# Kernel tuning notes

Measured on AMD Instinct MI355X. Metric: run time of the kernel, lower is better.

## Reference

```python
import jax, jax.numpy as jnp
import numpy as np

DEPTH = 256
SEQ = 394
EMB = 300


def _branch(x_nch, W, b, n):
    # W: [depth, n*EMB], flatten order of paragraph[i:i+n,:].flatten() is (time, emb)
    k = W.reshape(DEPTH, n, EMB).transpose(0, 2, 1)  # OIH: [depth, EMB, n]
    y = jax.lax.conv_general_dilated(
        x_nch, k, window_strides=(1,), padding='VALID',
        dimension_numbers=('NCH', 'OIH', 'NCH'))  # [B, depth, SEQ-n+1]
    # original loop only covers windows i = 0 .. SEQ-n-1 (SEQ-n windows)
    y = y[:, :, :SEQ - n] + b  # b: [depth, 1] broadcasts over time
    # running max starts at 0 and relu clamps >= 0; outer relu is a no-op
    return jnp.max(jax.nn.relu(y), axis=-1)  # [B, depth]


def setup_inputs() -> dict:
    key = jax.random.key(0)
    ks = jax.random.split(key, 7)
    inp = {
        'input': jax.random.normal(ks[0], (64, SEQ, EMB), dtype=jnp.float32),
        'W1': jax.random.normal(ks[1], (DEPTH, 3 * EMB), dtype=jnp.float32),
        'W2': jax.random.normal(ks[2], (DEPTH, 4 * EMB), dtype=jnp.float32),
        'W3': jax.random.normal(ks[3], (DEPTH, 5 * EMB), dtype=jnp.float32),
        'b1': jax.random.normal(ks[4], (DEPTH, 1), dtype=jnp.float32),
        'b2': jax.random.normal(ks[5], (DEPTH, 1), dtype=jnp.float32),
        'b3': jax.random.normal(ks[6], (DEPTH, 1), dtype=jnp.float32),
    }
    return inp


def reference(input, W1, W2, W3, b1, b2, b3):
    x = input.transpose(0, 2, 1)  # [B, EMB, SEQ] (NCH)
    o1 = _branch(x, W1, b1, 3)
    o2 = _branch(x, W2, b2, 4)
    o3 = _branch(x, W3, b3, 5)
    return jnp.concatenate([o1, o2, o3], axis=1)  # [B, 3*depth]
```

## Files before the change

kernel.cpp:

```cpp
#include <hip/hip_runtime.h>
#include <hip/hip_bf16.h>

#define SEQ 394
#define EMB 300
#define EMBP 312
#define NROWS (64 * SEQ)
#define XPTOT ((long)NROWS * EMBP)
#define NCHT 118
#define CBE0 29
#define CBE1 68
#define XELEM 41472

typedef __attribute__((ext_vector_type(8))) short short8;
typedef __attribute__((ext_vector_type(4))) float f32x4;

__device__ __forceinline__ unsigned short f2b(float f) {
    unsigned u = __float_as_uint(f);
    u += 0x7FFFu + ((u >> 16) & 1u);
    return (unsigned short)(u >> 16);
}

__device__ __forceinline__ void gload_lds16(const void* g, void* l) {
    __builtin_amdgcn_global_load_lds(
        (const __attribute__((address_space(1))) void*)g,
        (__attribute__((address_space(3))) void*)l, 16, 0, 0);
}


__global__ __launch_bounds__(256)
void pack_x_kernel(const float* __restrict__ x, unsigned short* __restrict__ xp)
{
    long q = (long)blockIdx.x * 256 + threadIdx.x;
    int row = (int)(q / 78);
    int c4  = ((int)(q - (long)row * 78)) * 4;
    ushort4 u;
    if (c4 < 300) {
        float4 v = *(const float4*)(x + (long)row * 300 + c4);
        u = make_ushort4(f2b(v.x), f2b(v.y), f2b(v.z), f2b(v.w));
    } else {
        u = make_ushort4(0, 0, 0, 0);
    }
    *(ushort4*)(xp + q * 4) = u;
}

__global__ __launch_bounds__(256)
void pack_w_kernel(const float* __restrict__ W1, const float* __restrict__ W2,
                   const float* __restrict__ W3, unsigned short* __restrict__ wb)
{
    int G = blockIdx.x * 256 + threadIdx.x;
    int l  = G & 63;
    int g  = (G >> 6) & 15;
    int c  = G >> 10;
    const float* Wg; int n, cb;
    if (c <= CBE0)      { Wg = W1; n = 3; cb = 0;        }
    else if (c <= CBE1) { Wg = W2; n = 4; cb = CBE0 + 1; }
    else                { Wg = W3; n = 5; cb = CBE1 + 1; }
    const int K = n * 300;
    const int f = g * 16 + (l & 15);
    const int kl = (c - cb) * 32 + (l >> 4) * 8;
    unsigned short v[8];
#pragma unroll
    for (int j = 0; j < 8; ++j) {
        int kk = kl + j;
        int r  = kk / EMBP;
        int e  = kk - r * EMBP;
        v[j] = (r < n && e < 300) ? f2b(Wg[(long)f * K + r * 300 + e]) : (unsigned short)0;
    }
    unsigned short* dst = wb + (long)G * 8;
    *(ushort4*)dst       = make_ushort4(v[0], v[1], v[2], v[3]);
    *(ushort4*)(dst + 4) = make_ushort4(v[4], v[5], v[6], v[7]);
}


__global__ __launch_bounds__(1024, 1)
void convgemm_kernel(const unsigned short* __restrict__ xp,
                     const unsigned short* __restrict__ wb,
                     const float* __restrict__ b1, const float* __restrict__ b2,
                     const float* __restrict__ b3,
                     float* __restrict__ out)
{
    __shared__ unsigned short X[XELEM];

    const int tid  = threadIdx.x;
    const int lane = tid & 63;
    const int wid  = tid >> 6;
    const int wfs  = wid >> 1;
    const int ws   = wid & 1;
    const int lr   = lane & 15, lg = lane >> 4;
    const int b    = blockIdx.x >> 2;
    const int ti   = blockIdx.x & 3;
    const int woff = (ti == 0) ? 0 : (ti == 1) ? 88 : (ti == 2) ? 176 : 263;

    {
        const long xbase = ((long)b * SEQ + woff) * EMBP;
        const long slim  = XPTOT - 8;
#pragma unroll
        for (int rd = 0; rd < 6; ++rd) {
            int gbase = rd * 1024 + wid * 64;
            if (gbase < 5184) {
                long se = xbase + (long)(gbase + lane) * 8;
                if (se > slim) se = slim;
                gload_lds16(xp + se, &X[gbase * 8]);
            }
        }
    }
    __syncthreads();

    const unsigned short* wp0 = wb + ((long)(wfs * 2) * 64 + lane) * 8;
    auto LDW = [&](int c, short8 (&w)[2]) {
        const short8* p = (const short8*)(wp0 + (long)c * 8192);
        w[0] = p[0];
        w[1] = p[64];
    };

    const unsigned short* xr = &X[(ws * 64 + lr) * EMBP + lg * 8];
    auto RDBX = [&](int ko, short8 (&bx)[4]) {
        bx[0] = *(const short8*)(xr + ko);
        bx[1] = *(const short8*)(xr + ko + 16 * EMBP);
        bx[2] = *(const short8*)(xr + ko + 32 * EMBP);
        bx[3] = *(const short8*)(xr + ko + 48 * EMBP);
    };

    auto MFMA8 = [&](const short8 (&w)[2], const short8 (&bx)[4], f32x4 (&acc)[2][4]) {
#pragma unroll
        for (int mi = 0; mi < 2; ++mi)
#pragma unroll
            for (int ni = 0; ni < 4; ++ni)
                acc[mi][ni] = __builtin_amdgcn_mfma_f32_16x16x32_bf16(w[mi], bx[ni], acc[mi][ni], 0, 0, 0);
    };

    auto EPI = [&](int br, f32x4 (&acc)[2][4]) {
        const float* bg = (br == 0) ? b1 : (br == 1) ? b2 : b3;
        const int Nw = 391 - br;
        const int ob = b * 768 + br * 256;
#pragma unroll
        for (int mi = 0; mi < 2; ++mi) {
#pragma unroll
            for (int r = 0; r < 4; ++r) {
                const int d = wfs * 32 + mi * 16 + lg * 4 + r;
                const float bv = bg[d];
                float m = 0.f;
#pragma unroll
                for (int ni = 0; ni < 4; ++ni) {
                    int w = woff + ws * 64 + ni * 16 + lr;
                    float v = fmaxf(acc[mi][ni][r] + bv, 0.f);
                    if (w >= Nw) v = 0.f;
                    m = fmaxf(m, v);
                }
#pragma unroll
                for (int off = 1; off < 16; off <<= 1)
                    m = fmaxf(m, __shfl_xor(m, off));
                if (lr == 0)
                    atomicMax((int*)(out + ob + d), __float_as_int(m));
            }
        }
#pragma unroll
        for (int i = 0; i < 2; ++i)
#pragma unroll
            for (int j = 0; j < 4; ++j)
                acc[i][j] = (f32x4)0.0f;
    };

    f32x4 accA[2][4], accB[2][4];
#pragma unroll
    for (int i = 0; i < 2; ++i)
#pragma unroll
        for (int j = 0; j < 4; ++j) {
            accA[i][j] = (f32x4)0.0f;
            accB[i][j] = (f32x4)0.0f;
        }

    short8 w1A[2], w1B[2], w2A[2], w2B[2], bx[4];

    LDW(30, w1A); LDW(69, w2A);
    LDW(31, w1B); LDW(70, w2B);
    for (int j = 0; j < 38; j += 2) {
        RDBX(j * 32, bx);
        MFMA8(w1A, bx, accA);
        MFMA8(w2A, bx, accB);
        { int t = (j + 2 < 39) ? j + 2 : 38; LDW(30 + t, w1A); LDW(69 + t, w2A); }

        RDBX((j + 1) * 32, bx);
        MFMA8(w1B, bx, accA);
        MFMA8(w2B, bx, accB);
        { int t = (j + 3 < 39) ? j + 3 : 38; LDW(30 + t, w1B); LDW(69 + t, w2B); }
    }
    RDBX(38 * 32, bx);
    MFMA8(w1A, bx, accA);
    MFMA8(w2A, bx, accB);

    LDW(69 + 39, w2A); LDW(69 + 40, w2B);
    EPI(1, accA);

    for (int t = 0; t < 10; t += 2) {
        RDBX((39 + t) * 32, bx);
        MFMA8(w2A, bx, accB);
        { int u = (41 + t < 49) ? 41 + t : 48; LDW(69 + u, w2A); }

        RDBX((40 + t) * 32, bx);
        MFMA8(w2B, bx, accB);
        { int u = (42 + t < 49) ? 42 + t : 48; LDW(69 + u, w2B); }
    }

    LDW(0, w1A); LDW(1, w1B);
    EPI(2, accB);

    for (int j = 0; j < 30; j += 2) {
        RDBX(j * 32, bx);
        MFMA8(w1A, bx, accA);
        { int t = (j + 2 < 30) ? j + 2 : 29; LDW(t, w1A); }

        RDBX((j + 1) * 32, bx);
        MFMA8(w1B, bx, accA);
        { int t = (j + 3 < 30) ? j + 3 : 29; LDW(t, w1B); }
    }
    EPI(0, accA);
}


__device__ __forceinline__ void load_chunk(const float* __restrict__ Wg,
                                           const float* __restrict__ xb,
                                           int K, int dbase, int i0, int k0, int tid,
                                           float4 wv[4], float4 xv[4])
{
#pragma unroll
    for (int i = 0; i < 4; ++i) {
        int fi  = tid + (i << 8);
        int row = fi >> 3;
        int c4  = (fi & 7) << 2;
        int col = k0 + c4;
        if (col < K)
            wv[i] = *(const float4*)(Wg + (long)(dbase + row) * K + col);
        else
            wv[i] = make_float4(0.f, 0.f, 0.f, 0.f);
        int off = (i0 + row) * EMB + col;
        int lim = SEQ * EMB - 4;
        if (off > lim) off = lim;
        xv[i] = *(const float4*)(xb + off);
    }
}

__device__ __forceinline__ void write_chunk(unsigned short (*Wb)[40],
                                            unsigned short (*Xb)[40],
                                            int tid, const float4 wv[4], const float4 xv[4])
{
#pragma unroll
    for (int i = 0; i < 4; ++i) {
        int fi  = tid + (i << 8);
        int row = fi >> 3;
        int c4  = (fi & 7) << 2;
        *(ushort4*)&Wb[row][c4] = make_ushort4(f2b(wv[i].x), f2b(wv[i].y), f2b(wv[i].z), f2b(wv[i].w));
        *(ushort4*)&Xb[row][c4] = make_ushort4(f2b(xv[i].x), f2b(xv[i].y), f2b(xv[i].z), f2b(xv[i].w));
    }
}

__global__ __launch_bounds__(256, 2)
void convmax_fallback(const float* __restrict__ x,
                      const float* __restrict__ W1, const float* __restrict__ W2,
                      const float* __restrict__ W3,
                      const float* __restrict__ b1, const float* __restrict__ b2,
                      const float* __restrict__ b3,
                      float* __restrict__ out)
{
    const int br = blockIdx.z;
    const int K  = (br == 0) ? 900 : (br == 1) ? 1200 : 1500;
    const int Nw = SEQ - 3 - br;
    const float* Wg = (br == 0) ? W1 : (br == 1) ? W2 : W3;
    const float* bg = (br == 0) ? b1 : (br == 1) ? b2 : b3;
    const int b  = blockIdx.x;
    const int mt = blockIdx.y >> 2;
    const int nt = blockIdx.y & 3;
    const int dbase = mt * 128;
    const int i0    = nt * 128;
    const float* xb = x + b * (SEQ * EMB);
    const int nch = (K + 31) >> 5;

    __shared__ unsigned short Wl[2][128][40];
    __shared__ unsigned short Xl[2][128][40];

    const int tid  = threadIdx.x;
    const int lane = tid & 63;
    const int wid  = tid >> 6;
    const int wr = wid >> 1, wc = wid & 1;
    const int lr = lane & 15, lg = lane >> 4;

    f32x4 acc[4][4];
#pragma unroll
    for (int i = 0; i < 4; ++i)
#pragma unroll
        for (int j = 0; j < 4; ++j)
            acc[i][j] = (f32x4)0.0f;

    {
        float4 wv[4], xv[4];
        load_chunk(Wg, xb, K, dbase, i0, 0, tid, wv, xv);
        write_chunk(Wl[0], Xl[0], tid, wv, xv);
    }
    __syncthreads();

    for (int c = 0; c < nch; ++c) {
        const int cur = c & 1;
        float4 wv[4], xv[4];
        const bool pf = (c + 1 < nch);
        if (pf) load_chunk(Wg, xb, K, dbase, i0, (c + 1) << 5, tid, wv, xv);

        short8 af[4], bfr[4];
#pragma unroll
        for (int mi = 0; mi < 4; ++mi)
            af[mi] = *(const short8*)&Wl[cur][wr * 64 + mi * 16 + lr][lg * 8];
#pragma unroll
        for (int ni = 0; ni < 4; ++ni)
            bfr[ni] = *(const short8*)&Xl[cur][wc * 64 + ni * 16 + lr][lg * 8];
#pragma unroll
        for (int mi = 0; mi < 4; ++mi)
#pragma unroll
            for (int ni = 0; ni < 4; ++ni)
                acc[mi][ni] = __builtin_amdgcn_mfma_f32_16x16x32_bf16(af[mi], bfr[ni], acc[mi][ni], 0, 0, 0);

        if (pf) write_chunk(Wl[cur ^ 1], Xl[cur ^ 1], tid, wv, xv);
        __syncthreads();
    }

    const int ob = b * 768 + br * 256;
#pragma unroll
    for (int mi = 0; mi < 4; ++mi) {
#pragma unroll
        for (int rI = 0; rI < 4; ++rI) {
            const int d = dbase + wr * 64 + mi * 16 + lg * 4 + rI;
            const float bv = bg[d];
            float m = 0.f;
#pragma unroll
            for (int ni = 0; ni < 4; ++ni) {
                int win = i0 + wc * 64 + ni * 16 + lr;
                float v = acc[mi][ni][rI] + bv;
                v = fmaxf(v, 0.f);
                if (win >= Nw) v = 0.f;
                m = fmaxf(m, v);
            }
#pragma unroll
            for (int off = 1; off < 16; off <<= 1)
                m = fmaxf(m, __shfl_xor(m, off));
            if (lr == 0)
                atomicMax((int*)(out + ob + d), __float_as_int(m));
        }
    }
}


extern "C" void kernel_launch(void* const* d_in, const int* in_sizes, int n_in,
                              void* d_out, int out_size, void* d_ws, size_t ws_size,
                              hipStream_t stream) {
    const float* x  = (const float*)d_in[0];
    const float* W1 = (const float*)d_in[1];
    const float* W2 = (const float*)d_in[2];
    const float* W3 = (const float*)d_in[3];
    const float* b1 = (const float*)d_in[4];
    const float* b2 = (const float*)d_in[5];
    const float* b3 = (const float*)d_in[6];
    float* out = (float*)d_out;

    hipMemsetAsync(d_out, 0, (size_t)out_size * sizeof(float), stream);

    const long WBTOT = (long)NCHT * 8192;
    const size_t need = (size_t)(XPTOT + WBTOT) * 2;

    if (ws_size >= need) {
        unsigned short* xp = (unsigned short*)d_ws;
        unsigned short* wbb = xp + XPTOT;

        pack_x_kernel<<<7683, 256, 0, stream>>>(x, xp);
        pack_w_kernel<<<472, 256, 0, stream>>>(W1, W2, W3, wbb);
        convgemm_kernel<<<256, 1024, 0, stream>>>(xp, wbb, b1, b2, b3, out);
    } else {
        dim3 grid(64, 8, 3);
        convmax_fallback<<<grid, 256, 0, stream>>>(x, W1, W2, W3, b1, b2, b3, out);
    }
}
```

Before: 85.00 us.

## Fuse input bf16 packing into conv GEMM and restructure MFMA software pipeline

```diff
diff --git a/kernel.cpp b/kernel.cpp
--- a/kernel.cpp
+++ b/kernel.cpp
@@ -5,11 +5,11 @@
 #define EMB 300
 #define EMBP 312
 #define NROWS (64 * SEQ)
-#define XPTOT ((long)NROWS * EMBP)
 #define NCHT 118
 #define CBE0 29
 #define CBE1 68
 #define XELEM 41472
+#define XGR 5148
 
 typedef __attribute__((ext_vector_type(8))) short short8;
 typedef __attribute__((ext_vector_type(4))) float f32x4;
@@ -20,28 +20,6 @@
     return (unsigned short)(u >> 16);
 }
 
-__device__ __forceinline__ void gload_lds16(const void* g, void* l) {
-    __builtin_amdgcn_global_load_lds(
-        (const __attribute__((address_space(1))) void*)g,
-        (__attribute__((address_space(3))) void*)l, 16, 0, 0);
-}
-
-
-__global__ __launch_bounds__(256)
-void pack_x_kernel(const float* __restrict__ x, unsigned short* __restrict__ xp)
-{
-    long q = (long)blockIdx.x * 256 + threadIdx.x;
-    int row = (int)(q / 78);
-    int c4  = ((int)(q - (long)row * 78)) * 4;
-    ushort4 u;
-    if (c4 < 300) {
-        float4 v = *(const float4*)(x + (long)row * 300 + c4);
-        u = make_ushort4(f2b(v.x), f2b(v.y), f2b(v.z), f2b(v.w));
-    } else {
-        u = make_ushort4(0, 0, 0, 0);
-    }
-    *(ushort4*)(xp + q * 4) = u;
-}
 
 __global__ __launch_bounds__(256)
 void pack_w_kernel(const float* __restrict__ W1, const float* __restrict__ W2,
@@ -73,7 +51,7 @@
 
 
 __global__ __launch_bounds__(1024, 1)
-void convgemm_kernel(const unsigned short* __restrict__ xp,
+void convgemm_kernel(const float* __restrict__ x,
                      const unsigned short* __restrict__ wb,
                      const float* __restrict__ b1, const float* __restrict__ b2,
                      const float* __restrict__ b3,
@@ -91,27 +69,42 @@
     const int ti   = blockIdx.x & 3;
     const int woff = (ti == 0) ? 0 : (ti == 1) ? 88 : (ti == 2) ? 176 : 263;
 
-    {
-        const long xbase = ((long)b * SEQ + woff) * EMBP;
-        const long slim  = XPTOT - 8;
-#pragma unroll
-        for (int rd = 0; rd < 6; ++rd) {
-            int gbase = rd * 1024 + wid * 64;
-            if (gbase < 5184) {
-                long se = xbase + (long)(gbase + lane) * 8;
-                if (se > slim) se = slim;
-                gload_lds16(xp + se, &X[gbase * 8]);
-            }
-        }
-    }
-    __syncthreads();
-
     const unsigned short* wp0 = wb + ((long)(wfs * 2) * 64 + lane) * 8;
     auto LDW = [&](int c, short8 (&w)[2]) {
         const short8* p = (const short8*)(wp0 + (long)c * 8192);
         w[0] = p[0];
         w[1] = p[64];
     };
+
+    short8 w1[2], w2[2];
+    LDW(30, w1); LDW(69, w2);
+
+    {
+        const float* xs = x + ((long)b * SEQ + woff) * 300;
+        const long growbase = (long)b * SEQ + woff;
+#pragma unroll
+        for (int rd = 0; rd < 6; ++rd) {
+            int gi = rd * 1024 + tid;
+            if (gi < XGR) {
+                int row = gi / 39;
+                int g   = gi - row * 39;
+                const float* src = xs + (long)gi * 8 - 12 * row;
+                float4 v0 = make_float4(0.f, 0.f, 0.f, 0.f);
+                float4 v1 = make_float4(0.f, 0.f, 0.f, 0.f);
+                if (growbase + row < NROWS) {
+                    if (g < 37) {
+                        v0 = *(const float4*)src;
+                        v1 = *(const float4*)(src + 4);
+                    } else if (g == 37) {
+                        v0 = *(const float4*)src;
+                    }
+                }
+                *(ushort4*)&X[gi * 8]     = make_ushort4(f2b(v0.x), f2b(v0.y), f2b(v0.z), f2b(v0.w));
+                *(ushort4*)&X[gi * 8 + 4] = make_ushort4(f2b(v1.x), f2b(v1.y), f2b(v1.z), f2b(v1.w));
+            }
+        }
+    }
+    __syncthreads();
 
     const unsigned short* xr = &X[(ws * 64 + lr) * EMBP + lg * 8];
     auto RDBX = [&](int ko, short8 (&bx)[4]) {
@@ -170,49 +163,69 @@
             accB[i][j] = (f32x4)0.0f;
         }
 
-    short8 w1A[2], w1B[2], w2A[2], w2B[2], bx[4];
-
-    LDW(30, w1A); LDW(69, w2A);
-    LDW(31, w1B); LDW(70, w2B);
+    short8 bxA[4], bxB[4];
+    RDBX(0, bxA);
+
     for (int j = 0; j < 38; j += 2) {
-        RDBX(j * 32, bx);
-        MFMA8(w1A, bx, accA);
-        MFMA8(w2A, bx, accB);
-        { int t = (j + 2 < 39) ? j + 2 : 38; LDW(30 + t, w1A); LDW(69 + t, w2A); }
-
-        RDBX((j + 1) * 32, bx);
-        MFMA8(w1B, bx, accA);
-        MFMA8(w2B, bx, accB);
-        { int t = (j + 3 < 39) ? j + 3 : 38; LDW(30 + t, w1B); LDW(69 + t, w2B); }
-    }
-    RDBX(38 * 32, bx);
-    MFMA8(w1A, bx, accA);
-    MFMA8(w2A, bx, accB);
-
-    LDW(69 + 39, w2A); LDW(69 + 40, w2B);
+        RDBX((j + 1) * 32, bxB);
+        __builtin_amdgcn_sched_barrier(0);
+        __builtin_amdgcn_s_setprio(1);
+        MFMA8(w1, bxA, accA);
+        MFMA8(w2, bxA, accB);
+        __builtin_amdgcn_s_setprio(0);
+        LDW(30 + j + 1, w1); LDW(69 + j + 1, w2);
+
+        RDBX((j + 2) * 32, bxA);
+        __builtin_amdgcn_sched_barrier(0);
+        __builtin_amdgcn_s_setprio(1);
+        MFMA8(w1, bxB, accA);
+        MFMA8(w2, bxB, accB);
+        __builtin_amdgcn_s_setprio(0);
+        LDW(30 + j + 2, w1); LDW(69 + j + 2, w2);
+    }
+    __builtin_amdgcn_s_setprio(1);
+    MFMA8(w1, bxA, accA);
+    MFMA8(w2, bxA, accB);
+    __builtin_amdgcn_s_setprio(0);
+
+    LDW(108, w2);
+    RDBX(39 * 32, bxB);
     EPI(1, accA);
 
-    for (int t = 0; t < 10; t += 2) {
-        RDBX((39 + t) * 32, bx);
-        MFMA8(w2A, bx, accB);
-        { int u = (41 + t < 49) ? 41 + t : 48; LDW(69 + u, w2A); }
-
-        RDBX((40 + t) * 32, bx);
-        MFMA8(w2B, bx, accB);
-        { int u = (42 + t < 49) ? 42 + t : 48; LDW(69 + u, w2B); }
-    }
-
-    LDW(0, w1A); LDW(1, w1B);
+    for (int u = 0; u < 10; u += 2) {
+        RDBX((40 + u) * 32, bxA);
+        __builtin_amdgcn_sched_barrier(0);
+        __builtin_amdgcn_s_setprio(1);
+        MFMA8(w2, bxB, accB);
+        __builtin_amdgcn_s_setprio(0);
+        LDW(109 + u, w2);
+
+        { int t = (41 + u <= 48) ? 41 + u : 48; RDBX(t * 32, bxB); }
+        __builtin_amdgcn_sched_barrier(0);
+        __builtin_amdgcn_s_setprio(1);
+        MFMA8(w2, bxA, accB);
+        __builtin_amdgcn_s_setprio(0);
+        { int t = (110 + u <= 117) ? 110 + u : 117; LDW(t, w2); }
+    }
+
+    LDW(0, w1);
+    RDBX(0, bxA);
     EPI(2, accB);
 
     for (int j = 0; j < 30; j += 2) {
-        RDBX(j * 32, bx);
-        MFMA8(w1A, bx, accA);
-        { int t = (j + 2 < 30) ? j + 2 : 29; LDW(t, w1A); }
-
-        RDBX((j + 1) * 32, bx);
-        MFMA8(w1B, bx, accA);
-        { int t = (j + 3 < 30) ? j + 3 : 29; LDW(t, w1B); }
+        RDBX((j + 1) * 32, bxB);
+        __builtin_amdgcn_sched_barrier(0);
+        __builtin_amdgcn_s_setprio(1);
+        MFMA8(w1, bxA, accA);
+        __builtin_amdgcn_s_setprio(0);
+        LDW(j + 1, w1);
+
+        { int t = (j + 2 <= 29) ? j + 2 : 29; RDBX(t * 32, bxA); }
+        __builtin_amdgcn_sched_barrier(0);
+        __builtin_amdgcn_s_setprio(1);
+        MFMA8(w1, bxB, accA);
+        __builtin_amdgcn_s_setprio(0);
+        { int t = (j + 2 <= 29) ? j + 2 : 29; LDW(t, w1); }
     }
     EPI(0, accA);
 }
@@ -361,16 +374,12 @@
 
     hipMemsetAsync(d_out, 0, (size_t)out_size * sizeof(float), stream);
 
-    const long WBTOT = (long)NCHT * 8192;
-    const size_t need = (size_t)(XPTOT + WBTOT) * 2;
+    const size_t need = (size_t)NCHT * 8192 * 2;
 
     if (ws_size >= need) {
-        unsigned short* xp = (unsigned short*)d_ws;
-        unsigned short* wbb = xp + XPTOT;
-
-        pack_x_kernel<<<7683, 256, 0, stream>>>(x, xp);
+        unsigned short* wbb = (unsigned short*)d_ws;
         pack_w_kernel<<<472, 256, 0, stream>>>(W1, W2, W3, wbb);
-        convgemm_kernel<<<256, 1024, 0, stream>>>(xp, wbb, b1, b2, b3, out);
+        convgemm_kernel<<<256, 1024, 0, stream>>>(x, wbb, b1, b2, b3, out);
     } else {
         dim3 grid(64, 8, 3);
         convmax_fallback<<<grid, 256, 0, stream>>>(x, W1, W2, W3, b1, b2, b3, out);
```

Result: faster. 80.61 us (-5.2%).
